# Kernel tuning notes

Hardware: AMD Instinct MI355X
Metric: run time of the kernel (lower is better)

The kernel has to match this reference:

```python
import jax, jax.numpy as jnp
import numpy as np

N, E, F_IN, F_E, EMB, G = 25000, 100000, 32, 8, 32, 512


def _nnconv(x, src, dst, ea, w1, b1, w2, b2, root, bias):
    # edge MLP: [E,F_E] -> [E,16] -> [E, in*EMB] -> per-edge weight matrix [E,in,EMB]
    h = jax.nn.relu(ea @ w1 + b1)
    W = (h @ w2 + b2).reshape(ea.shape[0], x.shape[1], EMB)
    # gather source nodes, per-edge matmul, scatter-add to targets (PyG NNConv, aggr='add')
    msg = jnp.einsum('ei,eio->eo', x[src], W)
    agg = jax.ops.segment_sum(msg, dst, num_segments=x.shape[0])
    return agg + x @ root + bias


def _branch(x, ei, ea, p0, p1):
    x = jax.nn.relu(_nnconv(x, ei[0], ei[1], ea, *p0))
    x = jax.nn.relu(_nnconv(x, ei[0], ei[1], ea, *p1))
    return x


def setup_inputs() -> dict:
    key = jax.random.key(0)
    ks = iter(jax.random.split(key, 64))
    def rnd(shape, s=1.0):
        return jax.random.normal(next(ks), shape, dtype=jnp.float32) * s
    inp = {
        'x_p': rnd((N, F_IN)), 'x_d': rnd((N, F_IN)),
        'edge_attr_p': rnd((E, F_E)), 'edge_attr_d': rnd((E, F_E)),
        'edge_index_p': jax.random.randint(next(ks), (2, E), 0, N),
        'edge_index_d': jax.random.randint(next(ks), (2, E), 0, N),
        'batch_p': jnp.sort(jax.random.randint(next(ks), (N,), 0, G)),
        'batch_d': jnp.sort(jax.random.randint(next(ks), (N,), 0, G)),
    }
    for b in ('p', 'd'):
        inp[b + '_nn0_w1'] = rnd((F_E, 16), 0.1)
        inp[b + '_nn0_b1'] = rnd((16,), 0.1)
        inp[b + '_nn0_w2'] = rnd((16, F_IN * EMB), 0.1)
        inp[b + '_nn0_b2'] = rnd((F_IN * EMB,), 0.1)
        inp[b + '_root0'] = rnd((F_IN, EMB), 0.1)
        inp[b + '_bias0'] = rnd((EMB,), 0.1)
        inp[b + '_nn1_w1'] = rnd((F_E, 16), 0.1)
        inp[b + '_nn1_b1'] = rnd((16,), 0.1)
        inp[b + '_nn1_w2'] = rnd((16, EMB * EMB), 0.1)
        inp[b + '_nn1_b2'] = rnd((EMB * EMB,), 0.1)
        inp[b + '_root1'] = rnd((EMB, EMB), 0.1)
        inp[b + '_bias1'] = rnd((EMB,), 0.1)
    inp['lin0_w'] = rnd((2 * EMB, 2 * EMB), 0.1)
    inp['lin0_b'] = rnd((2 * EMB,), 0.1)
    inp['lin1_w'] = rnd((2 * EMB, 1), 0.1)
    inp['lin1_b'] = rnd((1,), 0.1)
    return inp


def reference(x_p, x_d, edge_attr_p, edge_attr_d, edge_index_p, edge_index_d, batch_p, batch_d,
              p_nn0_w1, p_nn0_b1, p_nn0_w2, p_nn0_b2, p_root0, p_bias0,
              p_nn1_w1, p_nn1_b1, p_nn1_w2, p_nn1_b2, p_root1, p_bias1,
              d_nn0_w1, d_nn0_b1, d_nn0_w2, d_nn0_b2, d_root0, d_bias0,
              d_nn1_w1, d_nn1_b1, d_nn1_w2, d_nn1_b2, d_root1, d_bias1,
              lin0_w, lin0_b, lin1_w, lin1_b):
    p0 = (p_nn0_w1, p_nn0_b1, p_nn0_w2, p_nn0_b2, p_root0, p_bias0)
    p1 = (p_nn1_w1, p_nn1_b1, p_nn1_w2, p_nn1_b2, p_root1, p_bias1)
    d0 = (d_nn0_w1, d_nn0_b1, d_nn0_w2, d_nn0_b2, d_root0, d_bias0)
    d1 = (d_nn1_w1, d_nn1_b1, d_nn1_w2, d_nn1_b2, d_root1, d_bias1)
    hp = _branch(x_p, edge_index_p, edge_attr_p, p0, p1)      # [N, EMB]
    hd = _branch(x_d, edge_index_d, edge_attr_d, d0, d1)      # [N, EMB]
    gp = jax.ops.segment_max(hp, batch_p, num_segments=G)     # global_max_pool
    gd = jax.ops.segment_max(hd, batch_d, num_segments=G)
    x = jnp.concatenate([gp, gd], axis=1)                     # [G, 2*EMB]
    # F.dropout(p=0.5, training=False) is the identity in eval mode
    x = x @ lin0_w + lin0_b
    x = x @ lin1_w + lin1_b                                    # [G, 1]
    return x
```

## Files before the change

kernel.cpp:

```cpp
#include <hip/hip_runtime.h>
#include <hip/hip_bf16.h>

#define NN 25000
#define NE 100000
#define NG 512
#define NPAD 25024
#define NEP 100032
#define NT 6250
#define XL (2 * NPAD * 32)

typedef __attribute__((ext_vector_type(8))) short short8;
typedef __attribute__((ext_vector_type(4))) float f32x4;

__device__ __forceinline__ float bf2f(unsigned short u) {
    union { unsigned u; float f; } v; v.u = (unsigned)u << 16; return v.f;
}
__device__ __forceinline__ unsigned short f2bf(float f) {
    union { __hip_bfloat16 b; unsigned short u; } c;
    c.b = __float2bfloat16(f);
    return c.u;
}
__device__ __forceinline__ unsigned pk2(float lo, float hi) {
    __hip_bfloat162 h2;
    h2.x = __float2bfloat16(lo);
    h2.y = __float2bfloat16(hi);
    union { __hip_bfloat162 h; unsigned u; } c; c.h = h2; return c.u;
}

struct PrepArgs {
    const float* w2[4]; const float* b2[4];
    const float* x0[2];
};
#define S1 (4 * 17 * 1024)
#define S2V (2 * NN * 8)
#define S3 (2 * NN)
#define S4 (NG * 64 / 4)
__global__ __launch_bounds__(256) void prep_kernel(PrepArgs pa,
        unsigned short* __restrict__ Wt, unsigned short* __restrict__ xb,
        int* __restrict__ hist, float* __restrict__ gbuf) {
    int idx = blockIdx.x * 256 + threadIdx.x;
    if (idx < S1) {
        int L = idx / (17 * 1024);
        int r = idx % (17 * 1024);
        int s = r >> 10, o = (r >> 5) & 31, i = r & 31;
        float v = (s < 16) ? pa.w2[L][s * 1024 + i * 32 + o] : pa.b2[L][i * 32 + o];
        Wt[idx] = f2bf(v);
        return;
    }
    idx -= S1;
    if (idx < S2V) {
        int br = idx / (NN * 8);
        int q = idx % (NN * 8);
        float4 v = *(const float4*)(pa.x0[br] + (size_t)q * 4);
        unsigned* dst = (unsigned*)(xb + (size_t)br * NPAD * 32 + (size_t)q * 4);
        dst[0] = pk2(v.x, v.y);
        dst[1] = pk2(v.z, v.w);
        return;
    }
    idx -= S2V;
    if (idx < S3) { hist[idx] = 0; return; }
    idx -= S3;
    if (idx < S4) {
        float4 z = make_float4(0.f, 0.f, 0.f, 0.f);
        *(float4*)(gbuf + (size_t)idx * 4) = z;
    }
}

__global__ __launch_bounds__(256) void hist_kernel(const int* __restrict__ ep,
        const int* __restrict__ ed, int* __restrict__ hist, int* __restrict__ slot) {
    int idx = blockIdx.x * 256 + threadIdx.x;
    if (idx >= 2 * NE) return;
    int br = idx >= NE, e = idx - br * NE;
    const int* ei = br ? ed : ep;
    slot[idx] = atomicAdd(&hist[br * NN + ei[NE + e]], 1);
}

__global__ __launch_bounds__(1024) void scan_kernel(const int* __restrict__ hist,
        int* __restrict__ ptr) {
    int br = blockIdx.x, t = threadIdx.x;
    const int* h = hist + br * NN;
    int* p = ptr + br * (NN + 1);
    int base = t * 25;
    int loc[25]; int s = 0;
    if (base < NN) {
        #pragma unroll
        for (int j = 0; j < 25; ++j) { loc[j] = h[base + j]; s += loc[j]; }
    }
    int w = t >> 6, ln = t & 63;
    int v = s;
    #pragma unroll
    for (int d = 1; d < 64; d <<= 1) {
        int u = __shfl_up(v, d, 64);
        if (ln >= d) v += u;
    }
    __shared__ int wsum[16];
    if (ln == 63) wsum[w] = v;
    __syncthreads();
    if (t < 16) {
        int x = wsum[t];
        #pragma unroll
        for (int d = 1; d < 16; d <<= 1) {
            int u = __shfl_up(x, d, 16);
            if ((t & 15) >= d) x += u;
        }
        wsum[t] = x;
    }
    __syncthreads();
    int run = (w ? wsum[w - 1] : 0) + (v - s);
    if (base < NN) {
        #pragma unroll
        for (int j = 0; j < 25; ++j) { p[base + j] = run; run += loc[j]; }
    }
    if (t == 0) p[NN] = wsum[15];
}

struct EdgeArgs {
    const float* ea[2]; const int* eidx[2];
    const float* w1[2]; const float* b1[2];
};
__global__ __launch_bounds__(256, 2) void edge_kernel(EdgeArgs A, int L,
        const unsigned short* __restrict__ Wt,
        const unsigned short* __restrict__ xb,
        const int* __restrict__ ptr, const int* __restrict__ slot,
        unsigned short* __restrict__ msg) {
    __shared__ unsigned tr[4][256];
    int br = blockIdx.x >> 8;
    int bb = blockIdx.x & 255;
    const float* ea   = A.ea[br];
    const int*   eidx = A.eidx[br];
    const float* w1   = A.w1[br];
    const float* b1   = A.b1[br];
    const unsigned short* W  = Wt + (size_t)(br * 2 + L) * 17 * 1024;
    const unsigned short* xc = xb + (size_t)L * XL + (size_t)br * NPAD * 32;
    const int* pt = ptr + br * (NN + 1);
    const int* sl = slot + br * NE;
    unsigned short* mg = msg + (size_t)br * NEP * 32;

    int tid = threadIdx.x;
    int wv = tid >> 6, lane = tid & 63;
    int lr = lane & 15, kg = lane >> 4;

    short8 WA[17], WB[17];
    #pragma unroll
    for (int s = 0; s < 17; ++s) {
        WA[s] = *(const short8*)(W + (size_t)s * 1024 + lr * 32 + kg * 8);
        WB[s] = *(const short8*)(W + (size_t)s * 1024 + (16 + lr) * 32 + kg * 8);
    }
    float w1r[32], b1r[4];
    #pragma unroll
    for (int r = 0; r < 4; ++r) {
        b1r[r] = b1[kg * 4 + r];
        #pragma unroll
        for (int i = 0; i < 8; ++i) w1r[r * 8 + i] = w1[i * 16 + kg * 4 + r];
    }

    for (int t = bb * 4 + wv; t < NT; t += 1024) {
        int e = t * 16 + lr;
        int src = eidx[e];
        int rk = 0;
        if (kg == 0) rk = pt[eidx[NE + e]] + sl[e];

        short8 xs8 = *(const short8*)(xc + (size_t)src * 32 + kg * 8);
        float xf[8];
        #pragma unroll
        for (int j = 0; j < 8; ++j) xf[j] = bf2f((unsigned short)xs8[j]);

        float4 ea0 = *(const float4*)(ea + (size_t)e * 8);
        float4 ea1 = *(const float4*)(ea + (size_t)e * 8 + 4);
        float hreg[4];
        #pragma unroll
        for (int r = 0; r < 4; ++r) {
            float h = b1r[r];
            h += ea0.x * w1r[r * 8 + 0]; h += ea0.y * w1r[r * 8 + 1];
            h += ea0.z * w1r[r * 8 + 2]; h += ea0.w * w1r[r * 8 + 3];
            h += ea1.x * w1r[r * 8 + 4]; h += ea1.y * w1r[r * 8 + 5];
            h += ea1.z * w1r[r * 8 + 6]; h += ea1.w * w1r[r * 8 + 7];
            hreg[r] = fmaxf(h, 0.f);
        }

        f32x4 acc0 = {0.f, 0.f, 0.f, 0.f}, acc1 = {0.f, 0.f, 0.f, 0.f};
        #pragma unroll
        for (int s = 0; s < 17; ++s) {
            short8 y;
            if (s < 16) {
                float hs = __shfl(hreg[s & 3], lr + ((s >> 2) << 4), 64);
                union { unsigned u[4]; short8 v; } yy;
                yy.u[0] = pk2(hs * xf[0], hs * xf[1]);
                yy.u[1] = pk2(hs * xf[2], hs * xf[3]);
                yy.u[2] = pk2(hs * xf[4], hs * xf[5]);
                yy.u[3] = pk2(hs * xf[6], hs * xf[7]);
                y = yy.v;
            } else {
                y = xs8;
            }
            acc0 = __builtin_amdgcn_mfma_f32_16x16x32_bf16(WA[s], y, acc0, 0, 0, 0);
            acc1 = __builtin_amdgcn_mfma_f32_16x16x32_bf16(WB[s], y, acc1, 0, 0, 0);
        }
        tr[wv][lr * 16 + kg * 2    ] = pk2(acc0[0], acc0[1]);
        tr[wv][lr * 16 + kg * 2 + 1] = pk2(acc0[2], acc0[3]);
        tr[wv][lr * 16 + 8 + kg * 2    ] = pk2(acc1[0], acc1[1]);
        tr[wv][lr * 16 + 8 + kg * 2 + 1] = pk2(acc1[2], acc1[3]);
        int rkb = __shfl(rk, lane >> 2, 64);
        uint4 val = *(uint4*)&tr[wv][(lane >> 2) * 16 + (lane & 3) * 4];
        *(uint4*)(mg + (size_t)rkb * 32 + (lane & 3) * 8) = val;
    }
}

struct GatherArgs { const float* root[2]; const float* bias[2]; const int* batch[2]; };
template<int LAST>
__global__ __launch_bounds__(256) void gather_kernel(GatherArgs G,
        const int* __restrict__ ptr, const unsigned short* __restrict__ msg,
        const unsigned short* __restrict__ xin_, unsigned short* __restrict__ xout_,
        float* __restrict__ gbuf) {
    int gw = (blockIdx.x * 256 + threadIdx.x) >> 5;
    int l = threadIdx.x & 31;
    int br = gw >= NN, n = gw - br * NN;
    const int* p = ptr + br * (NN + 1);
    int lo = p[n], hi = p[n + 1];
    const unsigned short* m = msg + (size_t)br * NEP * 32;
    int sub = l >> 3;
    int q   = l & 7;
    float ps0 = 0.f, ps1 = 0.f, ps2 = 0.f, ps3 = 0.f;
    for (int j = lo + sub; j < hi; j += 4) {
        uint2 w = *(const uint2*)(m + (size_t)j * 32 + q * 4);
        ps0 += bf2f((unsigned short)(w.x & 0xffffu));
        ps1 += bf2f((unsigned short)(w.x >> 16));
        ps2 += bf2f((unsigned short)(w.y & 0xffffu));
        ps3 += bf2f((unsigned short)(w.y >> 16));
    }
    ps0 += __shfl_xor(ps0, 8, 64); ps0 += __shfl_xor(ps0, 16, 64);
    ps1 += __shfl_xor(ps1, 8, 64); ps1 += __shfl_xor(ps1, 16, 64);
    ps2 += __shfl_xor(ps2, 8, 64); ps2 += __shfl_xor(ps2, 16, 64);
    ps3 += __shfl_xor(ps3, 8, 64); ps3 += __shfl_xor(ps3, 16, 64);
    int srcl = l >> 2;
    float t0 = __shfl(ps0, srcl, 32);
    float t1 = __shfl(ps1, srcl, 32);
    float t2 = __shfl(ps2, srcl, 32);
    float t3 = __shfl(ps3, srcl, 32);
    int c = l & 3;
    float sum = (c & 2) ? ((c & 1) ? t3 : t2) : ((c & 1) ? t1 : t0);

    float xv = bf2f(xin_[(size_t)br * NPAD * 32 + (size_t)n * 32 + l]);
    const float* R = G.root[br];
    float rsum = 0.f;
    #pragma unroll
    for (int i = 0; i < 32; ++i) rsum += __shfl(xv, i, 32) * R[i * 32 + l];
    float v = fmaxf(sum + rsum + G.bias[br][l], 0.f);
    if (!LAST) {
        xout_[(size_t)br * NPAD * 32 + (size_t)n * 32 + l] = f2bf(v);
    } else {
        int g = G.batch[br][n];
        atomicMax((int*)&gbuf[(size_t)g * 64 + br * 32 + l], __float_as_int(v));
    }
}

__global__ __launch_bounds__(64) void final_mlp_kernel(
        const float* __restrict__ gbuf,
        const float* __restrict__ w0, const float* __restrict__ b0,
        const float* __restrict__ w1v, const float* __restrict__ b1v,
        float* __restrict__ out) {
    int g = blockIdx.x;
    int j = threadIdx.x;
    const float* xr = gbuf + (size_t)g * 64;
    float y = b0[j];
    for (int i = 0; i < 64; ++i) y += xr[i] * w0[i * 64 + j];
    float t = y * w1v[j];
    #pragma unroll
    for (int off = 32; off > 0; off >>= 1) t += __shfl_down(t, off, 64);
    if (j == 0) out[g] = t + b1v[0];
}

static size_t aln(size_t v) { return (v + 255) & ~(size_t)255; }

extern "C" void kernel_launch(void* const* d_in, const int* in_sizes, int n_in,
                              void* d_out, int out_size, void* d_ws, size_t ws_size,
                              hipStream_t stream) {
    (void)in_sizes; (void)n_in; (void)out_size; (void)ws_size;
    char* w = (char*)d_ws;
    unsigned short* Wt  = (unsigned short*)w; w += aln((size_t)S1 * 2);
    unsigned short* xb  = (unsigned short*)w; w += aln((size_t)2 * XL * 2);
    unsigned short* msg = (unsigned short*)w; w += aln((size_t)2 * NEP * 32 * 2);
    int* hist = (int*)w; w += aln((size_t)2 * NN * 4);
    int* ptr  = (int*)w; w += aln((size_t)2 * (NN + 1) * 4);
    int* slot = (int*)w; w += aln((size_t)2 * NE * 4);
    float* gbuf = (float*)w; w += aln((size_t)NG * 64 * 4);

    const int* ep = (const int*)d_in[4];
    const int* ed = (const int*)d_in[5];

    PrepArgs pa;
    for (int L4 = 0; L4 < 4; ++L4) {
        int base = 8 + (L4 >> 1) * 12 + (L4 & 1) * 6;
        pa.w2[L4] = (const float*)d_in[base + 2];
        pa.b2[L4] = (const float*)d_in[base + 3];
    }
    pa.x0[0] = (const float*)d_in[0];
    pa.x0[1] = (const float*)d_in[1];
    prep_kernel<<<(S1 + S2V + S3 + S4 + 255) / 256, 256, 0, stream>>>(pa, Wt, xb, hist, gbuf);

    hist_kernel<<<(2 * NE + 255) / 256, 256, 0, stream>>>(ep, ed, hist, slot);
    scan_kernel<<<2, 1024, 0, stream>>>(hist, ptr);

    EdgeArgs ea; GatherArgs ga;
    for (int br = 0; br < 2; ++br) {
        ea.ea[br]    = (const float*)d_in[2 + br];
        ea.eidx[br]  = (const int*)d_in[4 + br];
        ga.batch[br] = (const int*)d_in[6 + br];
    }
    for (int L = 0; L < 2; ++L) {
        for (int br = 0; br < 2; ++br) {
            int base = 8 + br * 12 + L * 6;
            ea.w1[br]   = (const float*)d_in[base + 0];
            ea.b1[br]   = (const float*)d_in[base + 1];
            ga.root[br] = (const float*)d_in[base + 4];
            ga.bias[br] = (const float*)d_in[base + 5];
        }
        edge_kernel<<<512, 256, 0, stream>>>(ea, L, Wt, xb, ptr, slot, msg);
        if (L == 0)
            gather_kernel<0><<<6250, 256, 0, stream>>>(ga, ptr, msg,
                xb, xb + (size_t)XL, gbuf);
        else
            gather_kernel<1><<<6250, 256, 0, stream>>>(ga, ptr, msg,
                xb + (size_t)XL, nullptr, gbuf);
    }

    final_mlp_kernel<<<NG, 64, 0, stream>>>(gbuf,
        (const float*)d_in[32], (const float*)d_in[33],
        (const float*)d_in[34], (const float*)d_in[35],
        (float*)d_out);
}
```

Before: 111.0 us.

## Fuse hist+scan, stage edge weights in LDS, replace atomic max pool with sorted segment max

Merges the histogram and scan kernels into one launch, where the last block to finish (found with an atomic counter) performs the CSR prefix scan. The edge kernel now copies pre-swizzled MFMA weight fragments and the edge-MLP weights into LDS instead of holding them in registers, and raises occupancy to 4 blocks per CU with twice as many blocks. The final layer writes bf16 node features, and a new kernel does global max pooling by binary-searching the sorted batch array, then runs the final MLP, replacing the atomicMax pooling and the separate MLP kernel. This saves launches and register pressure in exchange for a serial single-block scan, extra LDS traffic per MFMA, and a max pool that starts from 0 and so depends on inputs being post-ReLU.

```diff
diff --git a/kernel.cpp b/kernel.cpp
--- a/kernel.cpp
+++ b/kernel.cpp
@@ -8,6 +8,8 @@
 #define NEP 100032
 #define NT 6250
 #define XL (2 * NPAD * 32)
+#define WSZ 17408
+#define HB 782
 
 typedef __attribute__((ext_vector_type(8))) short short8;
 typedef __attribute__((ext_vector_type(4))) float f32x4;
@@ -27,23 +29,28 @@
     union { __hip_bfloat162 h; unsigned u; } c; c.h = h2; return c.u;
 }
 
+#define S1 (4 * WSZ)
+#define S2V (2 * NN * 8)
+#define S3 (2 * NN)
+
 struct PrepArgs {
     const float* w2[4]; const float* b2[4];
     const float* x0[2];
 };
-#define S1 (4 * 17 * 1024)
-#define S2V (2 * NN * 8)
-#define S3 (2 * NN)
-#define S4 (NG * 64 / 4)
 __global__ __launch_bounds__(256) void prep_kernel(PrepArgs pa,
         unsigned short* __restrict__ Wt, unsigned short* __restrict__ xb,
-        int* __restrict__ hist, float* __restrict__ gbuf) {
+        int* __restrict__ hist, int* __restrict__ done) {
     int idx = blockIdx.x * 256 + threadIdx.x;
     if (idx < S1) {
-        int L = idx / (17 * 1024);
-        int r = idx % (17 * 1024);
-        int s = r >> 10, o = (r >> 5) & 31, i = r & 31;
-        float v = (s < 16) ? pa.w2[L][s * 1024 + i * 32 + o] : pa.b2[L][i * 32 + o];
+        int k4 = idx / WSZ;
+        int r  = idx % WSZ;
+        int fs = r >> 9;
+        int lane = (r >> 3) & 63;
+        int j = r & 7;
+        int s = fs >> 1, half = fs & 1;
+        int o = half * 16 + (lane & 15);
+        int i = (lane >> 4) * 8 + j;
+        float v = (s < 16) ? pa.w2[k4][s * 1024 + i * 32 + o] : pa.b2[k4][i * 32 + o];
         Wt[idx] = f2bf(v);
         return;
     }
@@ -59,102 +66,95 @@
     }
     idx -= S2V;
     if (idx < S3) { hist[idx] = 0; return; }
-    idx -= S3;
-    if (idx < S4) {
-        float4 z = make_float4(0.f, 0.f, 0.f, 0.f);
-        *(float4*)(gbuf + (size_t)idx * 4) = z;
-    }
-}
-
-__global__ __launch_bounds__(256) void hist_kernel(const int* __restrict__ ep,
-        const int* __restrict__ ed, int* __restrict__ hist, int* __restrict__ slot) {
+    if (idx == S3) *done = 0;
+}
+
+struct HSArgs { const int* eidx[2]; };
+__global__ __launch_bounds__(256) void histscan_kernel(HSArgs A,
+        int* __restrict__ hist, int* __restrict__ slot, int* __restrict__ ptr,
+        int* __restrict__ done) {
     int idx = blockIdx.x * 256 + threadIdx.x;
-    if (idx >= 2 * NE) return;
-    int br = idx >= NE, e = idx - br * NE;
-    const int* ei = br ? ed : ep;
-    slot[idx] = atomicAdd(&hist[br * NN + ei[NE + e]], 1);
-}
-
-__global__ __launch_bounds__(1024) void scan_kernel(const int* __restrict__ hist,
-        int* __restrict__ ptr) {
-    int br = blockIdx.x, t = threadIdx.x;
-    const int* h = hist + br * NN;
-    int* p = ptr + br * (NN + 1);
-    int base = t * 25;
-    int loc[25]; int s = 0;
-    if (base < NN) {
-        #pragma unroll
-        for (int j = 0; j < 25; ++j) { loc[j] = h[base + j]; s += loc[j]; }
-    }
-    int w = t >> 6, ln = t & 63;
+    int tid = threadIdx.x;
+    if (idx < 2 * NE) {
+        int br = idx >= NE, e = idx - br * NE;
+        slot[idx] = atomicAdd(&hist[br * NN + A.eidx[br][NE + e]], 1);
+    }
+    __syncthreads();
+    __shared__ int lastflag;
+    __shared__ int ws4[4];
+    if (tid == 0) {
+        __threadfence();
+        int r = atomicAdd(done, 1);
+        lastflag = (r == HB - 1);
+    }
+    __syncthreads();
+    if (!lastflag) return;
+    int lt = tid & 127, brc = tid >> 7;
+    const int* h = hist + brc * NN;
+    int* p = ptr + brc * (NN + 1);
+    int base = lt * 196;
+    int s = 0;
+    for (int j = 0; j < 196; ++j) {
+        int ii = base + j;
+        if (ii < NN)
+            s += __hip_atomic_load(&h[ii], __ATOMIC_RELAXED, __HIP_MEMORY_SCOPE_AGENT);
+    }
+    int w = tid >> 6, ln = tid & 63;
     int v = s;
     #pragma unroll
     for (int d = 1; d < 64; d <<= 1) {
         int u = __shfl_up(v, d, 64);
         if (ln >= d) v += u;
     }
-    __shared__ int wsum[16];
-    if (ln == 63) wsum[w] = v;
+    if (ln == 63) ws4[w] = v;
     __syncthreads();
-    if (t < 16) {
-        int x = wsum[t];
-        #pragma unroll
-        for (int d = 1; d < 16; d <<= 1) {
-            int u = __shfl_up(x, d, 16);
-            if ((t & 15) >= d) x += u;
+    int off = (w & 1) ? ws4[w - 1] : 0;
+    int run = off + (v - s);
+    for (int j = 0; j < 196; ++j) {
+        int ii = base + j;
+        if (ii < NN) {
+            int hv = __hip_atomic_load(&h[ii], __ATOMIC_RELAXED, __HIP_MEMORY_SCOPE_AGENT);
+            p[ii] = run;
+            run += hv;
         }
-        wsum[t] = x;
-    }
-    __syncthreads();
-    int run = (w ? wsum[w - 1] : 0) + (v - s);
-    if (base < NN) {
-        #pragma unroll
-        for (int j = 0; j < 25; ++j) { p[base + j] = run; run += loc[j]; }
-    }
-    if (t == 0) p[NN] = wsum[15];
+    }
+    if (lt == 127) p[NN] = run;
 }
 
 struct EdgeArgs {
     const float* ea[2]; const int* eidx[2];
     const float* w1[2]; const float* b1[2];
 };
-__global__ __launch_bounds__(256, 2) void edge_kernel(EdgeArgs A, int L,
+__global__ __launch_bounds__(256, 4) void edge_kernel(EdgeArgs A, int L,
         const unsigned short* __restrict__ Wt,
         const unsigned short* __restrict__ xb,
         const int* __restrict__ ptr, const int* __restrict__ slot,
         unsigned short* __restrict__ msg) {
+    __shared__ unsigned short Wl[WSZ];
+    __shared__ float w1s[128];
+    __shared__ float b1s[16];
     __shared__ unsigned tr[4][256];
-    int br = blockIdx.x >> 8;
-    int bb = blockIdx.x & 255;
+    int br = blockIdx.x >> 9;
+    int bb = blockIdx.x & 511;
     const float* ea   = A.ea[br];
     const int*   eidx = A.eidx[br];
-    const float* w1   = A.w1[br];
-    const float* b1   = A.b1[br];
-    const unsigned short* W  = Wt + (size_t)(br * 2 + L) * 17 * 1024;
     const unsigned short* xc = xb + (size_t)L * XL + (size_t)br * NPAD * 32;
     const int* pt = ptr + br * (NN + 1);
     const int* sl = slot + br * NE;
     unsigned short* mg = msg + (size_t)br * NEP * 32;
 
     int tid = threadIdx.x;
+    const uint4* Wg = (const uint4*)(Wt + (size_t)(br * 2 + L) * WSZ);
+    for (int i2 = tid; i2 < WSZ / 8; i2 += 256) ((uint4*)Wl)[i2] = Wg[i2];
+    if (tid < 128) w1s[tid] = A.w1[br][tid];
+    if (tid < 16)  b1s[tid] = A.b1[br][tid];
+    __syncthreads();
+
     int wv = tid >> 6, lane = tid & 63;
     int lr = lane & 15, kg = lane >> 4;
-
-    short8 WA[17], WB[17];
-    #pragma unroll
-    for (int s = 0; s < 17; ++s) {
-        WA[s] = *(const short8*)(W + (size_t)s * 1024 + lr * 32 + kg * 8);
-        WB[s] = *(const short8*)(W + (size_t)s * 1024 + (16 + lr) * 32 + kg * 8);
-    }
-    float w1r[32], b1r[4];
-    #pragma unroll
-    for (int r = 0; r < 4; ++r) {
-        b1r[r] = b1[kg * 4 + r];
-        #pragma unroll
-        for (int i = 0; i < 8; ++i) w1r[r * 8 + i] = w1[i * 16 + kg * 4 + r];
-    }
-
-    for (int t = bb * 4 + wv; t < NT; t += 1024) {
+    const unsigned short* Wp = Wl + lane * 8;
+
+    for (int t = bb * 4 + wv; t < NT; t += 2048) {
         int e = t * 16 + lr;
         int src = eidx[e];
         int rk = 0;
@@ -170,11 +170,12 @@
         float hreg[4];
         #pragma unroll
         for (int r = 0; r < 4; ++r) {
-            float h = b1r[r];
-            h += ea0.x * w1r[r * 8 + 0]; h += ea0.y * w1r[r * 8 + 1];
-            h += ea0.z * w1r[r * 8 + 2]; h += ea0.w * w1r[r * 8 + 3];
-            h += ea1.x * w1r[r * 8 + 4]; h += ea1.y * w1r[r * 8 + 5];
-            h += ea1.z * w1r[r * 8 + 6]; h += ea1.w * w1r[r * 8 + 7];
+            int k = kg * 4 + r;
+            float h = b1s[k];
+            h += ea0.x * w1s[0 * 16 + k]; h += ea0.y * w1s[1 * 16 + k];
+            h += ea0.z * w1s[2 * 16 + k]; h += ea0.w * w1s[3 * 16 + k];
+            h += ea1.x * w1s[4 * 16 + k]; h += ea1.y * w1s[5 * 16 + k];
+            h += ea1.z * w1s[6 * 16 + k]; h += ea1.w * w1s[7 * 16 + k];
             hreg[r] = fmaxf(h, 0.f);
         }
 
@@ -193,8 +194,10 @@
             } else {
                 y = xs8;
             }
-            acc0 = __builtin_amdgcn_mfma_f32_16x16x32_bf16(WA[s], y, acc0, 0, 0, 0);
-            acc1 = __builtin_amdgcn_mfma_f32_16x16x32_bf16(WB[s], y, acc1, 0, 0, 0);
+            short8 wa = *(const short8*)(Wp + (2 * s) * 512);
+            short8 wb = *(const short8*)(Wp + (2 * s + 1) * 512);
+            acc0 = __builtin_amdgcn_mfma_f32_16x16x32_bf16(wa, y, acc0, 0, 0, 0);
+            acc1 = __builtin_amdgcn_mfma_f32_16x16x32_bf16(wb, y, acc1, 0, 0, 0);
         }
         tr[wv][lr * 16 + kg * 2    ] = pk2(acc0[0], acc0[1]);
         tr[wv][lr * 16 + kg * 2 + 1] = pk2(acc0[2], acc0[3]);
@@ -206,20 +209,17 @@
     }
 }
 
-struct GatherArgs { const float* root[2]; const float* bias[2]; const int* batch[2]; };
-template<int LAST>
+struct GatherArgs { const float* root[2]; const float* bias[2]; };
 __global__ __launch_bounds__(256) void gather_kernel(GatherArgs G,
         const int* __restrict__ ptr, const unsigned short* __restrict__ msg,
-        const unsigned short* __restrict__ xin_, unsigned short* __restrict__ xout_,
-        float* __restrict__ gbuf) {
+        const unsigned short* __restrict__ xin_, unsigned short* __restrict__ xout_) {
     int gw = (blockIdx.x * 256 + threadIdx.x) >> 5;
     int l = threadIdx.x & 31;
     int br = gw >= NN, n = gw - br * NN;
     const int* p = ptr + br * (NN + 1);
     int lo = p[n], hi = p[n + 1];
     const unsigned short* m = msg + (size_t)br * NEP * 32;
-    int sub = l >> 3;
-    int q   = l & 7;
+    int sub = l >> 3, q = l & 7;
     float ps0 = 0.f, ps1 = 0.f, ps2 = 0.f, ps3 = 0.f;
     for (int j = lo + sub; j < hi; j += 4) {
         uint2 w = *(const uint2*)(m + (size_t)j * 32 + q * 4);
@@ -246,28 +246,47 @@
     #pragma unroll
     for (int i = 0; i < 32; ++i) rsum += __shfl(xv, i, 32) * R[i * 32 + l];
     float v = fmaxf(sum + rsum + G.bias[br][l], 0.f);
-    if (!LAST) {
-        xout_[(size_t)br * NPAD * 32 + (size_t)n * 32 + l] = f2bf(v);
-    } else {
-        int g = G.batch[br][n];
-        atomicMax((int*)&gbuf[(size_t)g * 64 + br * 32 + l], __float_as_int(v));
-    }
-}
-
-__global__ __launch_bounds__(64) void final_mlp_kernel(
-        const float* __restrict__ gbuf,
-        const float* __restrict__ w0, const float* __restrict__ b0,
-        const float* __restrict__ w1v, const float* __restrict__ b1v,
-        float* __restrict__ out) {
+    xout_[(size_t)br * NPAD * 32 + (size_t)n * 32 + l] = f2bf(v);
+}
+
+struct SFArgs {
+    const int* batch[2];
+    const float* lw0; const float* lb0; const float* lw1; const float* lb1;
+};
+__global__ __launch_bounds__(256) void segmaxfinal_kernel(SFArgs S,
+        const unsigned short* __restrict__ x2, float* __restrict__ out) {
     int g = blockIdx.x;
-    int j = threadIdx.x;
-    const float* xr = gbuf + (size_t)g * 64;
-    float y = b0[j];
-    for (int i = 0; i < 64; ++i) y += xr[i] * w0[i * 64 + j];
-    float t = y * w1v[j];
-    #pragma unroll
-    for (int off = 32; off > 0; off >>= 1) t += __shfl_down(t, off, 64);
-    if (j == 0) out[g] = t + b1v[0];
+    __shared__ float red[256];
+    __shared__ float xg[64];
+    int o = threadIdx.x & 31, row = threadIdx.x >> 5;
+    for (int brc = 0; brc < 2; ++brc) {
+        const int* b = S.batch[brc];
+        int lo = 0, hi = NN;
+        while (lo < hi) { int mid = (lo + hi) >> 1; if (b[mid] < g) lo = mid + 1; else hi = mid; }
+        int s0 = lo;
+        hi = NN;
+        while (lo < hi) { int mid = (lo + hi) >> 1; if (b[mid] < g + 1) lo = mid + 1; else hi = mid; }
+        int s1 = lo;
+        const unsigned short* h = x2 + (size_t)brc * NPAD * 32;
+        float mv = 0.f;
+        for (int n = s0 + row; n < s1; n += 8) mv = fmaxf(mv, bf2f(h[(size_t)n * 32 + o]));
+        red[threadIdx.x] = mv; __syncthreads();
+        if (row < 4) red[threadIdx.x] = fmaxf(red[threadIdx.x], red[threadIdx.x + 128]);
+        __syncthreads();
+        if (row < 2) red[threadIdx.x] = fmaxf(red[threadIdx.x], red[threadIdx.x + 64]);
+        __syncthreads();
+        if (row == 0) xg[brc * 32 + o] = fmaxf(red[threadIdx.x], red[threadIdx.x + 32]);
+        __syncthreads();
+    }
+    if (threadIdx.x < 64) {
+        int j = threadIdx.x;
+        float y = S.lb0[j];
+        for (int i = 0; i < 64; ++i) y += xg[i] * S.lw0[i * 64 + j];
+        float t = y * S.lw1[j];
+        #pragma unroll
+        for (int off = 32; off > 0; off >>= 1) t += __shfl_down(t, off, 64);
+        if (j == 0) out[g] = t + S.lb1[0];
+    }
 }
 
 static size_t aln(size_t v) { return (v + 255) & ~(size_t)255; }
@@ -278,15 +297,12 @@
     (void)in_sizes; (void)n_in; (void)out_size; (void)ws_size;
     char* w = (char*)d_ws;
     unsigned short* Wt  = (unsigned short*)w; w += aln((size_t)S1 * 2);
-    unsigned short* xb  = (unsigned short*)w; w += aln((size_t)2 * XL * 2);
+    unsigned short* xb  = (unsigned short*)w; w += aln((size_t)3 * XL * 2);
     unsigned short* msg = (unsigned short*)w; w += aln((size_t)2 * NEP * 32 * 2);
     int* hist = (int*)w; w += aln((size_t)2 * NN * 4);
     int* ptr  = (int*)w; w += aln((size_t)2 * (NN + 1) * 4);
     int* slot = (int*)w; w += aln((size_t)2 * NE * 4);
-    float* gbuf = (float*)w; w += aln((size_t)NG * 64 * 4);
-
-    const int* ep = (const int*)d_in[4];
-    const int* ed = (const int*)d_in[5];
+    int* done = (int*)w; w += aln(256);
 
     PrepArgs pa;
     for (int L4 = 0; L4 < 4; ++L4) {
@@ -296,16 +312,17 @@
     }
     pa.x0[0] = (const float*)d_in[0];
     pa.x0[1] = (const float*)d_in[1];
-    prep_kernel<<<(S1 + S2V + S3 + S4 + 255) / 256, 256, 0, stream>>>(pa, Wt, xb, hist, gbuf);
-
-    hist_kernel<<<(2 * NE + 255) / 256, 256, 0, stream>>>(ep, ed, hist, slot);
-    scan_kernel<<<2, 1024, 0, stream>>>(hist, ptr);
+    prep_kernel<<<(S1 + S2V + S3 + 1 + 255) / 256, 256, 0, stream>>>(pa, Wt, xb, hist, done);
+
+    HSArgs hs;
+    hs.eidx[0] = (const int*)d_in[4];
+    hs.eidx[1] = (const int*)d_in[5];
+    histscan_kernel<<<HB, 256, 0, stream>>>(hs, hist, slot, ptr, done);
 
     EdgeArgs ea; GatherArgs ga;
     for (int br = 0; br < 2; ++br) {
-        ea.ea[br]    = (const float*)d_in[2 + br];
-        ea.eidx[br]  = (const int*)d_in[4 + br];
-        ga.batch[br] = (const int*)d_in[6 + br];
+        ea.ea[br]   = (const float*)d_in[2 + br];
+        ea.eidx[br] = (const int*)d_in[4 + br];
     }
     for (int L = 0; L < 2; ++L) {
         for (int br = 0; br < 2; ++br) {
@@ -315,17 +332,17 @@
             ga.root[br] = (const float*)d_in[base + 4];
             ga.bias[br] = (const float*)d_in[base + 5];
         }
-        edge_kernel<<<512, 256, 0, stream>>>(ea, L, Wt, xb, ptr, slot, msg);
-        if (L == 0)
-            gather_kernel<0><<<6250, 256, 0, stream>>>(ga, ptr, msg,
-                xb, xb + (size_t)XL, gbuf);
-        else
-            gather_kernel<1><<<6250, 256, 0, stream>>>(ga, ptr, msg,
-                xb + (size_t)XL, nullptr, gbuf);
-    }
-
-    final_mlp_kernel<<<NG, 64, 0, stream>>>(gbuf,
-        (const float*)d_in[32], (const float*)d_in[33],
-        (const float*)d_in[34], (const float*)d_in[35],
-        (float*)d_out);
-}
+        edge_kernel<<<1024, 256, 0, stream>>>(ea, L, Wt, xb, ptr, slot, msg);
+        gather_kernel<<<6250, 256, 0, stream>>>(ga, ptr, msg,
+            xb + (size_t)L * XL, xb + (size_t)(L + 1) * XL);
+    }
+
+    SFArgs sf;
+    sf.batch[0] = (const int*)d_in[6];
+    sf.batch[1] = (const int*)d_in[7];
+    sf.lw0 = (const float*)d_in[32];
+    sf.lb0 = (const float*)d_in[33];
+    sf.lw1 = (const float*)d_in[34];
+    sf.lb1 = (const float*)d_in[35];
+    segmaxfinal_kernel<<<NG, 256, 0, stream>>>(sf, xb + (size_t)2 * XL, (float*)d_out);
+}
```

Result: slower. 340.7 us (+207.1%).
